# Optimization experiments

Measured on AMD Instinct MI355X. Metric: run time of the kernel, lower is better.

Reference implementation:

```python
import jax, jax.numpy as jnp
import numpy as np

B, DX, DY = 64, 1024, 10

def setup_inputs() -> dict:
    key = jax.random.key(0)
    k1, k2 = jax.random.split(key)
    inputs = jax.random.normal(k1, (B, DX, DX), dtype=jnp.float32)
    rho = jax.random.normal(k2, (DX, DY, DX, DY), dtype=jnp.float32)
    return {"inputs": inputs, "rho": rho}

def reference(inputs, rho):
    # Original: rho_res = einsum('bik,klmn,bmo->bilon', inputs, rho, inputs)
    #           trace   = einsum('bijij->b', rho_res)   (full trace of rank-5 tensor)
    #           rho_y   = einsum('bijik->bjk', rho_res / trace)  (partial trace)
    # Equivalent without materializing the rank-5 intermediate:
    #   rho_y_un[b,j,k] = sum_{i,p,m} inputs[b,i,p] rho[p,j,m,k] inputs[b,m,i]
    #                   = sum_{m,p} (inputs @ inputs)[b,m,p] rho[p,j,m,k]
    #   trace[b] = sum_j rho_y_un[b,j,j]  (partial trace commutes with full trace)
    A = jnp.einsum('bmi,bip->bmp', inputs, inputs)          # [B, DX, DX]
    rho_y = jnp.einsum('bmp,pjmk->bjk', A, rho)             # [B, DY, DY]
    trace = jnp.trace(rho_y, axis1=-2, axis2=-1)            # [B]
    return rho_y / trace[:, None, None]
```

## Files before the change

### kernel.cpp

```cpp
#include <hip/hip_runtime.h>
#include <stdint.h>

#define DX 1024
#define NB 64
#define DY 10
#define NJK 100

typedef unsigned short ushort_t;
typedef __attribute__((ext_vector_type(8))) short short8;
typedef __attribute__((ext_vector_type(4))) float f32x4;
typedef __attribute__((ext_vector_type(16))) float f32x16;

#define VMCNT6 asm volatile("s_waitcnt vmcnt(6)" ::: "memory")
#define VMCNT5 asm volatile("s_waitcnt vmcnt(5)" ::: "memory")
#define VMCNT4 asm volatile("s_waitcnt vmcnt(4)" ::: "memory")
#define VMCNT0 asm volatile("s_waitcnt vmcnt(0)" ::: "memory")
#define LGKM0 asm volatile("s_waitcnt lgkmcnt(0)" ::: "memory")
#define CFENCE asm volatile("" ::: "memory")

__device__ __forceinline__ unsigned short f2bf(float f) {
  unsigned int u = __builtin_bit_cast(unsigned int, f);
  u += 0x7fffu + ((u >> 16) & 1u);
  return (unsigned short)(u >> 16);
}
__device__ __forceinline__ float bf2f(unsigned short h) {
  unsigned int u = ((unsigned int)h) << 16;
  return __builtin_bit_cast(float, u);
}
__device__ __forceinline__ void gload16(const void* g, void* l) {
  __builtin_amdgcn_global_load_lds((const __attribute__((address_space(1))) unsigned int*)g,
                                   (__attribute__((address_space(3))) unsigned int*)l, 16, 0, 0);
}

__launch_bounds__(256)
__global__ void p0_rho(const float* __restrict__ rho, ushort_t* __restrict__ R2,
                       float* __restrict__ S) {
  __shared__ ushort_t R_s[112 * 128];
  int p = blockIdx.x;
  int t = threadIdx.x;
  const float* rp = rho + (size_t)p * (DY * DX * DY);
  ushort_t* R2p = R2 + (size_t)p * (112 * 1024);
  int m = t >> 1, h = t & 1;

  for (int mc = 0; mc < 8; ++mc) {
    __syncthreads();
    float ssum = 0.f;
#pragma unroll
    for (int j = 0; j < DY; ++j) {
      const float* bj = rp + (size_t)j * (DX * DY) + (size_t)(mc * 128 + m) * DY;
      const float4 q = *(const float4*)(bj + h * 4);
      const float e = bj[8 + h];
      int rb = j * DY + h * 4;
      R_s[((rb + 0) * 128 + m) ^ (((rb + 0) & 15) << 3)] = f2bf(q.x);
      R_s[((rb + 1) * 128 + m) ^ (((rb + 1) & 15) << 3)] = f2bf(q.y);
      R_s[((rb + 2) * 128 + m) ^ (((rb + 2) & 15) << 3)] = f2bf(q.z);
      R_s[((rb + 3) * 128 + m) ^ (((rb + 3) & 15) << 3)] = f2bf(q.w);
      int r8 = j * DY + 8 + h;
      R_s[(r8 * 128 + m) ^ ((r8 & 15) << 3)] = f2bf(e);
      if (h == 0) {
        if (j == 0) ssum += q.x;
        if (j == 1) ssum += q.y;
        if (j == 2) ssum += q.z;
        if (j == 3) ssum += q.w;
        if (j == 8) ssum += e;
      } else {
        if (j == 4) ssum += q.x;
        if (j == 5) ssum += q.y;
        if (j == 6) ssum += q.z;
        if (j == 7) ssum += q.w;
        if (j == 9) ssum += e;
      }
    }
    ssum += __shfl_xor(ssum, 1, 64);
    if (h == 0) S[(size_t)p * DX + mc * 128 + m] = ssum;
    __syncthreads();
#pragma unroll
    for (int i = 0; i < 7; ++i) {
      int c = i * 256 + t;
      int row = c >> 4, sl = c & 15;
      uint4 v = make_uint4(0u, 0u, 0u, 0u);
      if (row < NJK) v = *(const uint4*)&R_s[(row * 128 + sl * 8) ^ ((row & 15) << 3)];
      *(uint4*)(R2p + (size_t)row * 1024 + mc * 128 + sl * 8) = v;
    }
  }
}

__launch_bounds__(256)
__global__ void p0_split(const float* __restrict__ X,
                         ushort_t* __restrict__ XHL, ushort_t* __restrict__ XtHL) {
  __shared__ float T[64][65];
  int blk = blockIdx.x;
  int bl = blk >> 8;
  int tt = blk & 255;
  int r0 = (tt >> 4) << 6;
  int c0 = (tt & 15) << 6;
  const float* Xb = X + (size_t)bl * DX * DX;
  int t = threadIdx.x;
  int r = t >> 4, c = t & 15;
#pragma unroll
  for (int s = 0; s < 4; ++s) {
    const float4 v = *(const float4*)(Xb + (size_t)(r0 + r + 16 * s) * DX + c0 + c * 4);
    T[r + 16 * s][c * 4 + 0] = v.x;
    T[r + 16 * s][c * 4 + 1] = v.y;
    T[r + 16 * s][c * 4 + 2] = v.z;
    T[r + 16 * s][c * 4 + 3] = v.w;
  }
  __syncthreads();
  int s8 = t & 7;
  int rw = t >> 3;
  int isLo = s8 >> 2, q = s8 & 3;
#pragma unroll
  for (int ktl = 0; ktl < 2; ++ktl) {
#pragma unroll
    for (int sp = 0; sp < 2; ++sp) {
      int loc = rw + sp * 32;
      {
        unsigned short hh8[8];
#pragma unroll
        for (int e = 0; e < 8; ++e) {
          float x = T[loc][ktl * 32 + q * 8 + e];
          unsigned short hh = f2bf(x);
          hh8[e] = isLo ? f2bf(x - bf2f(hh)) : hh;
        }
        int kt = (c0 >> 5) + ktl;
        size_t off = (((size_t)bl * 32 + kt) * 1024 + (r0 + loc)) * 64 + s8 * 8;
        uint4 v;
        v.x = (unsigned)hh8[0] | ((unsigned)hh8[1] << 16);
        v.y = (unsigned)hh8[2] | ((unsigned)hh8[3] << 16);
        v.z = (unsigned)hh8[4] | ((unsigned)hh8[5] << 16);
        v.w = (unsigned)hh8[6] | ((unsigned)hh8[7] << 16);
        *(uint4*)(XHL + off) = v;
      }
      {
        unsigned short hh8[8];
#pragma unroll
        for (int e = 0; e < 8; ++e) {
          float x = T[ktl * 32 + q * 8 + e][loc];
          unsigned short hh = f2bf(x);
          hh8[e] = isLo ? f2bf(x - bf2f(hh)) : hh;
        }
        int kt = (r0 >> 5) + ktl;
        size_t off = (((size_t)bl * 32 + kt) * 1024 + (c0 + loc)) * 64 + s8 * 8;
        uint4 v;
        v.x = (unsigned)hh8[0] | ((unsigned)hh8[1] << 16);
        v.y = (unsigned)hh8[2] | ((unsigned)hh8[3] << 16);
        v.z = (unsigned)hh8[4] | ((unsigned)hh8[5] << 16);
        v.w = (unsigned)hh8[6] | ((unsigned)hh8[7] << 16);
        *(uint4*)(XtHL + off) = v;
      }
    }
  }
}

__launch_bounds__(512, 2)
__global__ void k1_gemm(const ushort_t* __restrict__ XHL,
                        const ushort_t* __restrict__ XtHL,
                        const float* __restrict__ S,
                        ushort_t* __restrict__ Ahg,
                        float* __restrict__ part_tr, int bg) {
  __shared__ ushort_t lds[65536];
  int wg = blockIdx.x;
  int cpx = gridDim.x >> 3;
  int gt = (wg & 7) * cpx + (wg >> 3);
  int bl = gt >> 4, tile = gt & 15;
  int b = bg + bl;
  int m0 = (tile >> 2) << 8, p0 = (tile & 3) << 8;
  int t = threadIdx.x;
  int wv = t >> 6, lane = t & 63, l31 = lane & 31, hi8 = lane >> 5;
  int wm = (wv >> 2) << 7, wp = (wv & 3) << 6;

  f32x16 acc[4][2];
#pragma unroll
  for (int mi = 0; mi < 4; ++mi)
#pragma unroll
    for (int ni = 0; ni < 2; ++ni)
#pragma unroll
      for (int e = 0; e < 16; ++e) acc[mi][ni][e] = 0.f;

  int lam = lane >> 3;
  int lsl = (lane & 7) ^ lam;
  const ushort_t* Asrc = XHL + ((size_t)bl * 32 * 1024 + m0) * 64 + (size_t)lsl * 8;
  const ushort_t* Bsrc = XtHL + ((size_t)bl * 32 * 1024 + p0) * 64 + (size_t)lsl * 8;
  int ldsw = (t & ~63) * 8;

  auto stageA = [&](int kt) {
    int buf = (kt & 1) << 15;
    size_t ko = (size_t)kt * 65536;
#pragma unroll
    for (int i = 0; i < 4; ++i) {
      int rr = (i << 6) + (wv << 3) + lam;
      gload16(Asrc + ko + (size_t)rr * 64, &lds[buf + (i << 12) + ldsw]);
    }
  };
  auto stageB = [&](int kt) {
    int buf = (kt & 1) << 15;
    size_t ko = (size_t)kt * 65536;
#pragma unroll
    for (int i = 0; i < 4; ++i) {
      int rr = (i << 6) + (wv << 3) + lam;
      gload16(Bsrc + ko + (size_t)rr * 64, &lds[buf + 16384 + (i << 12) + ldsw]);
    }
  };
  auto readB = [&](int buf, int kc, short8* bh, short8* blo) {
#pragma unroll
    for (int ni = 0; ni < 2; ++ni) {
      int p = wp + (ni << 5) + l31;
      int rowb = buf + 16384 + p * 64;
      bh[ni] = *(const short8*)&lds[rowb + (((kc * 2 + hi8) ^ (p & 7)) << 3)];
      blo[ni] = *(const short8*)&lds[rowb + (((4 + kc * 2 + hi8) ^ (p & 7)) << 3)];
    }
  };
  auto readA = [&](int buf, int kc, int mh, short8* ah, short8* al) {
#pragma unroll
    for (int mi2 = 0; mi2 < 2; ++mi2) {
      int m = wm + ((mh * 2 + mi2) << 5) + l31;
      int rowa = buf + m * 64;
      ah[mi2] = *(const short8*)&lds[rowa + (((kc * 2 + hi8) ^ (m & 7)) << 3)];
      al[mi2] = *(const short8*)&lds[rowa + (((4 + kc * 2 + hi8) ^ (m & 7)) << 3)];
    }
  };
  auto mfma12 = [&](int mh, const short8* ah, const short8* al,
                    const short8* bh, const short8* blo) {
    __builtin_amdgcn_s_setprio(1);
#pragma unroll
    for (int mi2 = 0; mi2 < 2; ++mi2) {
      int mi = mh * 2 + mi2;
#pragma unroll
      for (int ni = 0; ni < 2; ++ni) {
        acc[mi][ni] = __builtin_amdgcn_mfma_f32_32x32x16_bf16(ah[mi2], bh[ni], acc[mi][ni], 0, 0, 0);
        acc[mi][ni] = __builtin_amdgcn_mfma_f32_32x32x16_bf16(ah[mi2], blo[ni], acc[mi][ni], 0, 0, 0);
        acc[mi][ni] = __builtin_amdgcn_mfma_f32_32x32x16_bf16(al[mi2], bh[ni], acc[mi][ni], 0, 0, 0);
      }
    }
    __builtin_amdgcn_s_setprio(0);
  };

  stageA(0);
  stageB(0);
  VMCNT0;
  __builtin_amdgcn_s_barrier();

#pragma unroll 1
  for (int kt = 0; kt < 32; ++kt) {
    int buf = (kt & 1) << 15;
    short8 bh[2], blo[2], ah[2], al[2];
    readB(buf, 0, bh, blo);
    readA(buf, 0, 0, ah, al);
    if (kt < 31) stageA(kt + 1);
    CFENCE;
    __builtin_amdgcn_s_barrier();
    LGKM0;
    __builtin_amdgcn_sched_barrier(0);
    mfma12(0, ah, al, bh, blo);
    readA(buf, 0, 1, ah, al);
    if (kt < 31) stageB(kt + 1);
    CFENCE;
    __builtin_amdgcn_s_barrier();
    LGKM0;
    __builtin_amdgcn_sched_barrier(0);
    mfma12(1, ah, al, bh, blo);
    readB(buf, 1, bh, blo);
    readA(buf, 1, 0, ah, al);
    VMCNT4;
    CFENCE;
    __builtin_amdgcn_s_barrier();
    LGKM0;
    __builtin_amdgcn_sched_barrier(0);
    mfma12(0, ah, al, bh, blo);
    readA(buf, 1, 1, ah, al);
    VMCNT0;
    CFENCE;
    __builtin_amdgcn_s_barrier();
    LGKM0;
    __builtin_amdgcn_sched_barrier(0);
    mfma12(1, ah, al, bh, blo);
  }

  float tracc = 0.f;
#pragma unroll
  for (int mi = 0; mi < 4; ++mi)
#pragma unroll
    for (int ni = 0; ni < 2; ++ni) {
      int p = p0 + wp + (ni << 5) + l31;
#pragma unroll
      for (int rg = 0; rg < 4; ++rg) {
        int m = m0 + wm + (mi << 5) + 8 * rg + 4 * hi8;
        const float4 sv = *(const float4*)(S + (size_t)p * DX + m);
        tracc += acc[mi][ni][rg * 4 + 0] * sv.x + acc[mi][ni][rg * 4 + 1] * sv.y +
                 acc[mi][ni][rg * 4 + 2] * sv.z + acc[mi][ni][rg * 4 + 3] * sv.w;
      }
    }
#pragma unroll
  for (int off = 32; off > 0; off >>= 1) tracc += __shfl_xor(tracc, off, 64);
  __syncthreads();
  if (lane == 0) ((float*)lds)[wv] = tracc;
  __syncthreads();
  if (t == 0) {
    float s = 0.f;
    for (int i = 0; i < 8; ++i) s += ((float*)lds)[i];
    part_tr[b * 16 + tile] = s;
  }
  __syncthreads();

#pragma unroll
  for (int mi = 0; mi < 4; ++mi)
#pragma unroll
    for (int ni = 0; ni < 2; ++ni) {
      int p = wp + (ni << 5) + l31;
#pragma unroll
      for (int rg = 0; rg < 4; ++rg) {
        int m = wm + (mi << 5) + 8 * rg + 4 * hi8;
        unsigned int h0 = f2bf(acc[mi][ni][rg * 4 + 0]);
        unsigned int h1 = f2bf(acc[mi][ni][rg * 4 + 1]);
        unsigned int h2 = f2bf(acc[mi][ni][rg * 4 + 2]);
        unsigned int h3 = f2bf(acc[mi][ni][rg * 4 + 3]);
        int idx = p * 256 + (((m >> 3) ^ (p & 7)) << 3) + (m & 7);
        *(uint2*)&lds[idx] = make_uint2(h0 | (h1 << 16), h2 | (h3 << 16));
      }
    }
  __syncthreads();
#pragma unroll
  for (int i = 0; i < 16; ++i) {
    int cc = i * 512 + t;
    int row = cc >> 5, sl = cc & 31;
    int idx = row * 256 + ((sl ^ (row & 7)) << 3);
    uint4 v = *(const uint4*)&lds[idx];
    *(uint4*)(Ahg + ((size_t)(p0 + row) * NB + b) * DX + m0 + sl * 8) = v;
  }
}

__launch_bounds__(256)
__global__ void k2_contract(const ushort_t* __restrict__ R2,
                            const ushort_t* __restrict__ Ahg,
                            float* __restrict__ part_rho) {
  __shared__ ushort_t lds[22528];
  int p = blockIdx.x;
  int t = threadIdx.x;
  int wv = t >> 6, lane = t & 63, lr = lane & 15, lg = lane >> 4;
  const ushort_t* R2p = R2 + (size_t)p * (112 * 1024);
  const ushort_t* Ahp = Ahg + (size_t)p * (NB * DX);

  f32x4 acc[7];
#pragma unroll
  for (int n = 0; n < 7; ++n)
#pragma unroll
    for (int i = 0; i < 4; ++i) acc[n][i] = 0.f;

  auto stage = [&](int mc) {
    int buf = (mc & 1) * 11264;
#pragma unroll
    for (int i = 0; i < 2; ++i) {
      int c = i * 256 + t;
      int br = c >> 3, sl = c & 7;
      int lsl = sl ^ (br & 7);
      gload16(Ahp + (size_t)br * DX + mc * 64 + lsl * 8,
              &lds[buf + (i * 256 + (t & ~63)) * 8]);
    }
#pragma unroll
    for (int i = 0; i < 4; ++i) {
      int c = i * 256 + t;
      if (c < 896) {
        int row = c >> 3, sl = c & 7;
        int lsl = sl ^ (row & 7);
        gload16(R2p + (size_t)row * 1024 + mc * 64 + lsl * 8,
                &lds[buf + 4096 + (i * 256 + (t & ~63)) * 8]);
      }
    }
  };

  stage(0);
#pragma unroll 1
  for (int mc = 0; mc < 16; ++mc) {
    int buf = (mc & 1) * 11264;
    if (mc < 15) {
      stage(mc + 1);
      if (wv < 2) { VMCNT6; } else { VMCNT5; }
    } else {
      VMCNT0;
    }
    __builtin_amdgcn_s_barrier();
    CFENCE;
#pragma unroll
    for (int s = 0; s < 2; ++s) {
      int slot = s * 4 + lg;
      int ra = 16 * wv + lr;
      short8 af = *(const short8*)&lds[buf + ra * 64 + ((slot ^ (ra & 7)) << 3)];
      __builtin_amdgcn_s_setprio(1);
#pragma unroll
      for (int n = 0; n < 7; ++n) {
        int rb = 16 * n + lr;
        short8 bf = *(const short8*)&lds[buf + 4096 + rb * 64 + ((slot ^ (rb & 7)) << 3)];
        acc[n] = __builtin_amdgcn_mfma_f32_16x16x32_bf16(af, bf, acc[n], 0, 0, 0);
      }
      __builtin_amdgcn_s_setprio(0);
    }
    CFENCE;
    __builtin_amdgcn_s_barrier();
  }
#pragma unroll
  for (int n = 0; n < 7; ++n) {
    int col = 16 * n + lr;
    if (col < NJK) {
#pragma unroll
      for (int i = 0; i < 4; ++i) {
        int b_ = 16 * wv + lg * 4 + i;
        part_rho[((size_t)p * NB + b_) * NJK + col] = acc[n][i];
      }
    }
  }
}

__launch_bounds__(128)
__global__ void k3a(const float* __restrict__ part_rho, float* __restrict__ ws2) {
  int blk = blockIdx.x;
  int b = blk >> 1, h = blk & 1;
  int t = threadIdx.x;
  if (t >= NJK) return;
  float s = 0.f;
  for (int pp = 0; pp < 512; ++pp)
    s += part_rho[((size_t)(h * 512 + pp) * NB + b) * NJK + t];
  ws2[(size_t)(h * NB + b) * 128 + t] = s;
}

__launch_bounds__(128)
__global__ void k3b(const float* __restrict__ ws2, const float* __restrict__ part_tr,
                    float* __restrict__ out) {
  int b = blockIdx.x;
  int t = threadIdx.x;
  float tr = 0.f;
#pragma unroll
  for (int i = 0; i < 16; ++i) tr += part_tr[b * 16 + i];
  if (t < NJK) {
    float v = ws2[(size_t)b * 128 + t] + ws2[(size_t)(NB + b) * 128 + t];
    out[b * NJK + t] = v / tr;
  }
}

extern "C" void kernel_launch(void* const* d_in, const int* in_sizes, int n_in,
                              void* d_out, int out_size, void* d_ws, size_t ws_size,
                              hipStream_t stream) {
  const float* X = (const float*)d_in[0];
  const float* rho = (const float*)d_in[1];
  float* out = (float*)d_out;
  char* ws = (char*)d_ws;

  const size_t MB = 1048576ull;
  const size_t need_big = 868 * MB + 65536;
  const size_t need_small = 484 * MB + 65536;

  if (ws_size >= need_big) {
    ushort_t* XHL = (ushort_t*)(ws);
    ushort_t* XtHL = (ushort_t*)(ws + 256 * MB);
    ushort_t* Ahg = (ushort_t*)(ws + 512 * MB);
    ushort_t* R2 = (ushort_t*)(ws + 640 * MB);
    float* S = (float*)(ws + 864 * MB);
    float* part_tr = (float*)(ws + 868 * MB);
    float* part_rho = (float*)(ws);
    float* ws2 = (float*)(ws + 32 * MB);

    hipLaunchKernelGGL(p0_rho, dim3(1024), dim3(256), 0, stream, rho, R2, S);
    hipLaunchKernelGGL(p0_split, dim3(16384), dim3(256), 0, stream, X, XHL, XtHL);
    hipLaunchKernelGGL(k1_gemm, dim3(1024), dim3(512), 0, stream, XHL, XtHL, S, Ahg, part_tr, 0);
    hipLaunchKernelGGL(k2_contract, dim3(1024), dim3(256), 0, stream, R2, Ahg, part_rho);
    hipLaunchKernelGGL(k3a, dim3(128), dim3(128), 0, stream, part_rho, ws2);
    hipLaunchKernelGGL(k3b, dim3(64), dim3(128), 0, stream, ws2, part_tr, out);
  } else {
    ushort_t* XHL = (ushort_t*)(ws);
    ushort_t* XtHL = (ushort_t*)(ws + 64 * MB);
    ushort_t* Ahg = (ushort_t*)(ws + 128 * MB);
    ushort_t* R2 = (ushort_t*)(ws + 256 * MB);
    float* S = (float*)(ws + 480 * MB);
    float* part_tr = (float*)(ws + 484 * MB);
    float* part_rho = (float*)(ws);
    float* ws2 = (float*)(ws + 32 * MB);
    if (ws_size < need_small) return;

    hipLaunchKernelGGL(p0_rho, dim3(1024), dim3(256), 0, stream, rho, R2, S);
    for (int g = 0; g < 4; ++g) {
      hipLaunchKernelGGL(p0_split, dim3(4096), dim3(256), 0, stream,
                         X + (size_t)g * 16 * DX * DX, XHL, XtHL);
      hipLaunchKernelGGL(k1_gemm, dim3(256), dim3(512), 0, stream, XHL, XtHL, S, Ahg, part_tr, g * 16);
    }
    hipLaunchKernelGGL(k2_contract, dim3(1024), dim3(256), 0, stream, R2, Ahg, part_rho);
    hipLaunchKernelGGL(k3a, dim3(128), dim3(128), 0, stream, part_rho, ws2);
    hipLaunchKernelGGL(k3b, dim3(64), dim3(128), 0, stream, ws2, part_tr, out);
  }
}
```

Measured before the change: 737.6 us.

## Split GEMM k-loop into finer eight-phase pipeline with smaller MFMA groups

Restructures the main bf16 GEMM loop from four phases of 12 MFMAs into eight phases of 6 MFMAs. Each phase reads one A fragment pair instead of two, and global-to-LDS staging is split into half-stages interleaved across phases. The aim is finer overlap of LDS reads, global prefetch and MFMA work, with lower register pressure. In exchange it doubles the number of workgroup barriers per k-tile, which adds synchronisation overhead.

```diff
diff --git a/kernel.cpp b/kernel.cpp
--- a/kernel.cpp
+++ b/kernel.cpp
@@ -183,20 +183,20 @@
   const ushort_t* Bsrc = XtHL + ((size_t)bl * 32 * 1024 + p0) * 64 + (size_t)lsl * 8;
   int ldsw = (t & ~63) * 8;
 
-  auto stageA = [&](int kt) {
+  auto stageA2 = [&](int kt, int half) {
     int buf = (kt & 1) << 15;
     size_t ko = (size_t)kt * 65536;
 #pragma unroll
-    for (int i = 0; i < 4; ++i) {
+    for (int i = half * 2; i < half * 2 + 2; ++i) {
       int rr = (i << 6) + (wv << 3) + lam;
       gload16(Asrc + ko + (size_t)rr * 64, &lds[buf + (i << 12) + ldsw]);
     }
   };
-  auto stageB = [&](int kt) {
+  auto stageB2 = [&](int kt, int half) {
     int buf = (kt & 1) << 15;
     size_t ko = (size_t)kt * 65536;
 #pragma unroll
-    for (int i = 0; i < 4; ++i) {
+    for (int i = half * 2; i < half * 2 + 2; ++i) {
       int rr = (i << 6) + (wv << 3) + lam;
       gload16(Bsrc + ko + (size_t)rr * 64, &lds[buf + 16384 + (i << 12) + ldsw]);
     }
@@ -210,70 +210,67 @@
       blo[ni] = *(const short8*)&lds[rowb + (((4 + kc * 2 + hi8) ^ (p & 7)) << 3)];
     }
   };
-  auto readA = [&](int buf, int kc, int mh, short8* ah, short8* al) {
-#pragma unroll
-    for (int mi2 = 0; mi2 < 2; ++mi2) {
-      int m = wm + ((mh * 2 + mi2) << 5) + l31;
-      int rowa = buf + m * 64;
-      ah[mi2] = *(const short8*)&lds[rowa + (((kc * 2 + hi8) ^ (m & 7)) << 3)];
-      al[mi2] = *(const short8*)&lds[rowa + (((4 + kc * 2 + hi8) ^ (m & 7)) << 3)];
-    }
-  };
-  auto mfma12 = [&](int mh, const short8* ah, const short8* al,
-                    const short8* bh, const short8* blo) {
+  auto readA2 = [&](int buf, int kc, int mi, short8& a, short8& l) {
+    int m = wm + (mi << 5) + l31;
+    int rowa = buf + m * 64;
+    a = *(const short8*)&lds[rowa + (((kc * 2 + hi8) ^ (m & 7)) << 3)];
+    l = *(const short8*)&lds[rowa + (((4 + kc * 2 + hi8) ^ (m & 7)) << 3)];
+  };
+  auto mfma6 = [&](int mi, const short8& a, const short8& l,
+                   const short8* bh, const short8* blo) {
     __builtin_amdgcn_s_setprio(1);
 #pragma unroll
-    for (int mi2 = 0; mi2 < 2; ++mi2) {
-      int mi = mh * 2 + mi2;
-#pragma unroll
-      for (int ni = 0; ni < 2; ++ni) {
-        acc[mi][ni] = __builtin_amdgcn_mfma_f32_32x32x16_bf16(ah[mi2], bh[ni], acc[mi][ni], 0, 0, 0);
-        acc[mi][ni] = __builtin_amdgcn_mfma_f32_32x32x16_bf16(ah[mi2], blo[ni], acc[mi][ni], 0, 0, 0);
-        acc[mi][ni] = __builtin_amdgcn_mfma_f32_32x32x16_bf16(al[mi2], bh[ni], acc[mi][ni], 0, 0, 0);
-      }
+    for (int ni = 0; ni < 2; ++ni) {
+      acc[mi][ni] = __builtin_amdgcn_mfma_f32_32x32x16_bf16(a, bh[ni], acc[mi][ni], 0, 0, 0);
+      acc[mi][ni] = __builtin_amdgcn_mfma_f32_32x32x16_bf16(a, blo[ni], acc[mi][ni], 0, 0, 0);
+      acc[mi][ni] = __builtin_amdgcn_mfma_f32_32x32x16_bf16(l, bh[ni], acc[mi][ni], 0, 0, 0);
     }
     __builtin_amdgcn_s_setprio(0);
   };
 
-  stageA(0);
-  stageB(0);
+  stageA2(0, 0);
+  stageA2(0, 1);
+  stageB2(0, 0);
+  stageB2(0, 1);
   VMCNT0;
   __builtin_amdgcn_s_barrier();
 
 #pragma unroll 1
   for (int kt = 0; kt < 32; ++kt) {
     int buf = (kt & 1) << 15;
-    short8 bh[2], blo[2], ah[2], al[2];
+    short8 bh[2], blo[2], a, l;
     readB(buf, 0, bh, blo);
-    readA(buf, 0, 0, ah, al);
-    if (kt < 31) stageA(kt + 1);
-    CFENCE;
-    __builtin_amdgcn_s_barrier();
-    LGKM0;
-    __builtin_amdgcn_sched_barrier(0);
-    mfma12(0, ah, al, bh, blo);
-    readA(buf, 0, 1, ah, al);
-    if (kt < 31) stageB(kt + 1);
-    CFENCE;
-    __builtin_amdgcn_s_barrier();
-    LGKM0;
-    __builtin_amdgcn_sched_barrier(0);
-    mfma12(1, ah, al, bh, blo);
+    readA2(buf, 0, 0, a, l);
+    if (kt < 31) stageA2(kt + 1, 0);
+    CFENCE; __builtin_amdgcn_s_barrier(); LGKM0; __builtin_amdgcn_sched_barrier(0);
+    mfma6(0, a, l, bh, blo);
+    readA2(buf, 0, 1, a, l);
+    if (kt < 31) stageA2(kt + 1, 1);
+    CFENCE; __builtin_amdgcn_s_barrier(); LGKM0; __builtin_amdgcn_sched_barrier(0);
+    mfma6(1, a, l, bh, blo);
+    readA2(buf, 0, 2, a, l);
+    if (kt < 31) stageB2(kt + 1, 0);
+    CFENCE; __builtin_amdgcn_s_barrier(); LGKM0; __builtin_amdgcn_sched_barrier(0);
+    mfma6(2, a, l, bh, blo);
+    readA2(buf, 0, 3, a, l);
+    if (kt < 31) stageB2(kt + 1, 1);
+    CFENCE; __builtin_amdgcn_s_barrier(); LGKM0; __builtin_amdgcn_sched_barrier(0);
+    mfma6(3, a, l, bh, blo);
     readB(buf, 1, bh, blo);
-    readA(buf, 1, 0, ah, al);
-    VMCNT4;
-    CFENCE;
-    __builtin_amdgcn_s_barrier();
-    LGKM0;
-    __builtin_amdgcn_sched_barrier(0);
-    mfma12(0, ah, al, bh, blo);
-    readA(buf, 1, 1, ah, al);
+    readA2(buf, 1, 0, a, l);
+    CFENCE; __builtin_amdgcn_s_barrier(); LGKM0; __builtin_amdgcn_sched_barrier(0);
+    mfma6(0, a, l, bh, blo);
+    readA2(buf, 1, 1, a, l);
+    if (kt < 31) { VMCNT4; }
+    CFENCE; __builtin_amdgcn_s_barrier(); LGKM0; __builtin_amdgcn_sched_barrier(0);
+    mfma6(1, a, l, bh, blo);
+    readA2(buf, 1, 2, a, l);
+    CFENCE; __builtin_amdgcn_s_barrier(); LGKM0; __builtin_amdgcn_sched_barrier(0);
+    mfma6(2, a, l, bh, blo);
+    readA2(buf, 1, 3, a, l);
     VMCNT0;
-    CFENCE;
-    __builtin_amdgcn_s_barrier();
-    LGKM0;
-    __builtin_amdgcn_sched_barrier(0);
-    mfma12(1, ah, al, bh, blo);
+    CFENCE; __builtin_amdgcn_s_barrier(); LGKM0; __builtin_amdgcn_sched_barrier(0);
+    mfma6(3, a, l, bh, blo);
   }
 
   float tracc = 0.f;
```

After: 730.8 us. About the same (-0.9%).
